# Optimization experiments

Measured on AMD Instinct MI355X. Metric: run time of the kernel, lower is better.

The kernel has to match this reference:

```python
import jax, jax.numpy as jnp
import numpy as np

EMBED_DIM = 512
SE_HIDDEN = max(1, int(EMBED_DIM * 0.25))  # 128
LN_EPS = 1e-5


def setup_inputs() -> dict:
    key = jax.random.key(0)
    ks = jax.random.split(key, 16)
    B, H, W, D = 8, 32, 32, EMBED_DIM
    s = 0.02
    return {
        "q": jax.random.normal(ks[0], (B, H, W, D), jnp.float32),
        "k": jax.random.normal(ks[1], (B, H, W, D), jnp.float32),
        "v": jax.random.normal(ks[2], (B, H, W, D), jnp.float32),
        # Linear weights stored as [in, out] (equivalent to torch W.T)
        "Wq": jax.random.normal(ks[3], (D, D), jnp.float32) * s,
        "Wk": jax.random.normal(ks[4], (D, D), jnp.float32) * s,
        "Wv": jax.random.normal(ks[5], (D, D), jnp.float32) * s,
        "Wo": jax.random.normal(ks[6], (D, D), jnp.float32) * s,
        # Conv2d kernel in HWIO layout for NHWC conv
        "conv_w": jax.random.normal(ks[7], (3, 3, D, D), jnp.float32) * s,
        "conv_b": jnp.zeros((D,), jnp.float32),
        "se_w1": jax.random.normal(ks[8], (D, SE_HIDDEN), jnp.float32) * s,
        "se_b1": jnp.zeros((SE_HIDDEN,), jnp.float32),
        "se_w2": jax.random.normal(ks[9], (SE_HIDDEN, D), jnp.float32) * s,
        "se_b2": jnp.zeros((D,), jnp.float32),
        "ln_g": jnp.ones((D,), jnp.float32),
        "ln_b": jnp.zeros((D,), jnp.float32),
    }


def _layernorm(x, g, b):
    mu = jnp.mean(x, axis=-1, keepdims=True)
    var = jnp.mean(jnp.square(x - mu), axis=-1, keepdims=True)
    return (x - mu) * jax.lax.rsqrt(var + LN_EPS) * g + b


def reference(q, k, v, Wq, Wk, Wv, Wo, conv_w, conv_b,
              se_w1, se_b1, se_w2, se_b2, ln_g, ln_b):
    B, H, W, D = q.shape
    scaler = jnp.sqrt(jnp.asarray(D, q.dtype))
    qp = q @ Wq  # [B,H,W,D]
    kp = k @ Wk
    vp = v @ Wv
    N = H * W
    qf = qp.reshape(B, N, D)
    kf = kp.reshape(B, N, D)
    vf = vp.reshape(B, N, D)
    scores = jnp.einsum('bnd,bmd->bnm', qf, kf) / scaler
    probs = jax.nn.softmax(scores, axis=-1)  # dropout p=0 -> identity
    out = jnp.einsum('bnm,bmd->bnd', probs, vf).reshape(B, H, W, D)
    out = out @ Wo
    # 3x3 same conv in NHWC
    out = jax.lax.conv_general_dilated(
        out, conv_w, window_strides=(1, 1), padding='SAME',
        dimension_numbers=('NHWC', 'HWIO', 'NHWC')) + conv_b
    # squeeze-excite: global average pool over spatial dims
    se = jnp.mean(out, axis=(1, 2))  # [B,D]
    se = jax.nn.silu(se @ se_w1 + se_b1)
    se = jax.nn.sigmoid(se @ se_w2 + se_b2)  # [B,D]
    out = out * se[:, None, None, :]
    x = qp + out  # residual uses q AFTER q_proj (q reassigned in torch code)
    return _layernorm(x, ln_g, ln_b)
```

## Files before the change

### kernel.cpp

```cpp
#include <hip/hip_runtime.h>
#include <hip/hip_bf16.h>

using bf16 = __hip_bfloat16;
typedef __attribute__((ext_vector_type(8))) short short8;
typedef __attribute__((ext_vector_type(4))) short short4v;
typedef __attribute__((ext_vector_type(4))) float f32x4;

static const size_t OFF_QP   = 0;
static const size_t OFF_KP   = (size_t)8  << 20;
static const size_t OFF_VPT  = (size_t)16 << 20;
static const size_t OFF_SC   = (size_t)24 << 20;
static const size_t OFF_WT   = (size_t)56 << 20;
static const size_t OFF_CWT  = (size_t)58 << 20;
static const size_t OFF_POOL = (size_t)63 << 20;
static const size_t OFF_SE   = ((size_t)63 << 20) + 16384;

__global__ __launch_bounds__(256) void prep_k(const float* __restrict__ Wq,
                                              const float* __restrict__ Wk,
                                              const float* __restrict__ Wv,
                                              const float* __restrict__ Wo,
                                              const float* __restrict__ convw,
                                              bf16* __restrict__ wT,
                                              bf16* __restrict__ cwT,
                                              float* __restrict__ pooled) {
    long idx = (long)blockIdx.x * 256 + threadIdx.x;
    if (idx < 4l * 262144) {
        int m = (int)(idx >> 18);
        int o = (int)(idx & 262143);
        int n = o >> 9, k = o & 511;
        const float* W = (m == 0) ? Wq : (m == 1) ? Wk : (m == 2) ? Wv : Wo;
        wT[idx] = __float2bfloat16(W[k * 512 + n]);
    } else if (idx < 4l * 262144 + 512l * 4608) {
        long o = idx - 4l * 262144;
        int co = (int)(o / 4608), t = (int)(o % 4608);
        cwT[o] = __float2bfloat16(convw[(long)t * 512 + co]);
    } else if (idx < 4l * 262144 + 512l * 4608 + 4096) {
        pooled[idx - (4l * 262144 + 512l * 4608)] = 0.f;
    }
}

template <int OP>
__global__ __launch_bounds__(256, 2) void gemm_k(
    const void* __restrict__ Ap0, const void* __restrict__ Ap1, const void* __restrict__ Ap2,
    int lda, long sA,
    const bf16* __restrict__ BT, int ldb, long sB,
    void* __restrict__ Cp, int ldc, long sC,
    int K, const float* __restrict__ bias) {
    __shared__ bf16 As[2][128 * 64];
    __shared__ bf16 Bs[2][64 * 64];
    const int tid = threadIdx.x;
    const int l = tid & 63, w = tid >> 6;
    const int wm = w >> 1, wn = w & 1;

    const int gx = gridDim.x, gy = gridDim.y;
    const int nwg = gx * gy * gridDim.z;
    const int bid = blockIdx.x + gx * (blockIdx.y + gy * blockIdx.z);
    const int swz = (bid & 7) * (nwg >> 3) + (bid >> 3);
    const int bx = swz % gx;
    const int rem = swz / gx;
    const int by = rem % gy;
    const int zb = rem / gy;

    const int m0 = by * 128, n0 = bx * 64;
    const float isc = 0.04419417382415922f;

    const bf16* Ab = nullptr;
    const float* Af = nullptr;
    if (OP == 1) {
        Af = (const float*)(zb == 0 ? Ap0 : zb == 1 ? Ap1 : Ap2);
    } else {
        Ab = (const bf16*)Ap0 + (long)zb * sA;
    }
    const bf16* Bb = BT + (OP == 1 ? (long)zb * 262144 : (long)zb * sB);

    const int fr = l & 15;
    f32x4 acc[4][2] = {};

    int pixoff[4], hh_[4], wp_[4];
    if (OP == 3) {
#pragma unroll
        for (int i = 0; i < 4; ++i) {
            int s = tid + i * 256;
            int row = s >> 3, c = s & 7;
            int p = m0 + row;
            int bb = p >> 10;
            hh_[i] = (p >> 5) & 31;
            wp_[i] = p & 31;
            pixoff[i] = ((bb * 32 + hh_[i]) * 32 + wp_[i]) * 512 + c * 8;
        }
    }

    short8 ar[4];
    float4 af0[4], af1[4];
    short8 br[2];

    auto stage_load = [&](int t) {
        int k0 = t * 64;
        int dy = 0, dx = 0, doff = 0;
        if (OP == 3) {
            int tap = k0 >> 9;
            dy = tap / 3 - 1;
            dx = tap % 3 - 1;
            doff = (dy * 32 + dx) * 512 + (k0 & 511);
        }
#pragma unroll
        for (int i = 0; i < 4; ++i) {
            int s = tid + i * 256;
            int row = s >> 3, c = s & 7;
            if (OP == 1) {
                const float* src = Af + (long)(m0 + row) * lda + k0 + c * 8;
                af0[i] = *(const float4*)src;
                af1[i] = *(const float4*)(src + 4);
            } else if (OP == 3) {
                int h2 = hh_[i] + dy, w2 = wp_[i] + dx;
                if (((unsigned)h2 < 32u) & ((unsigned)w2 < 32u)) {
                    ar[i] = *(const short8*)(Ab + pixoff[i] + doff);
                } else {
                    short8 zz = {0, 0, 0, 0, 0, 0, 0, 0};
                    ar[i] = zz;
                }
            } else {
                ar[i] = *(const short8*)(Ab + (long)(m0 + row) * lda + k0 + c * 8);
            }
        }
#pragma unroll
        for (int i = 0; i < 2; ++i) {
            int s = tid + i * 256;
            int row = s >> 3, c = s & 7;
            br[i] = *(const short8*)(Bb + (long)(n0 + row) * ldb + k0 + c * 8);
        }
    };

    auto stage_write = [&](int b) {
#pragma unroll
        for (int i = 0; i < 4; ++i) {
            int s = tid + i * 256;
            int row = s >> 3, c = s & 7;
            int cx = c ^ (row & 7);
            if (OP == 1) {
                union { short8 s8; bf16 h[8]; } u;
                u.h[0] = __float2bfloat16(af0[i].x); u.h[1] = __float2bfloat16(af0[i].y);
                u.h[2] = __float2bfloat16(af0[i].z); u.h[3] = __float2bfloat16(af0[i].w);
                u.h[4] = __float2bfloat16(af1[i].x); u.h[5] = __float2bfloat16(af1[i].y);
                u.h[6] = __float2bfloat16(af1[i].z); u.h[7] = __float2bfloat16(af1[i].w);
                *(short8*)(&As[b][row * 64 + cx * 8]) = u.s8;
            } else {
                *(short8*)(&As[b][row * 64 + cx * 8]) = ar[i];
            }
        }
#pragma unroll
        for (int i = 0; i < 2; ++i) {
            int s = tid + i * 256;
            int row = s >> 3, c = s & 7;
            int cx = c ^ (row & 7);
            *(short8*)(&Bs[b][row * 64 + cx * 8]) = br[i];
        }
    };

    auto compute = [&](int b) {
#pragma unroll
        for (int h = 0; h < 2; ++h) {
            int cx = ((l >> 4) + 4 * h) ^ (fr & 7);
            short8 afr[4], bfv[2];
#pragma unroll
            for (int m = 0; m < 4; ++m) {
                int r = wm * 64 + m * 16 + fr;
                afr[m] = *(const short8*)(&As[b][r * 64 + cx * 8]);
            }
#pragma unroll
            for (int n = 0; n < 2; ++n) {
                int r = wn * 32 + n * 16 + fr;
                bfv[n] = *(const short8*)(&Bs[b][r * 64 + cx * 8]);
            }
#pragma unroll
            for (int m = 0; m < 4; ++m)
#pragma unroll
                for (int n = 0; n < 2; ++n)
                    acc[m][n] = __builtin_amdgcn_mfma_f32_16x16x32_bf16(afr[m], bfv[n], acc[m][n], 0, 0, 0);
        }
    };

    const int nt = K >> 6;
    stage_load(0);
    stage_write(0);
    int cur = 0;
    for (int t = 0; t < nt; ++t) {
        __syncthreads();
        if (t + 1 < nt) stage_load(t + 1);
        compute(cur);
        if (t + 1 < nt) stage_write(cur ^ 1);
        cur ^= 1;
    }

    const int cr = (l >> 4) * 4, cc = l & 15;
#pragma unroll
    for (int m = 0; m < 4; ++m) {
#pragma unroll
        for (int n = 0; n < 2; ++n) {
#pragma unroll
            for (int j = 0; j < 4; ++j) {
                int r = m0 + wm * 64 + m * 16 + cr + j;
                int c = n0 + wn * 32 + n * 16 + cc;
                float vv = acc[m][n][j];
                if (OP == 3) vv += bias[c];
                if (OP == 0 || OP == 2) {
                    ((bf16*)Cp)[(long)zb * sC + (long)r * ldc + c] = __float2bfloat16(vv);
                } else if (OP == 3) {
                    ((float*)Cp)[(long)zb * sC + (long)r * ldc + c] = vv;
                } else {
                    if (zb == 2) {
                        ((bf16*)Cp)[(size_t)(OFF_VPT / 2) + ((long)(r >> 10) * 512 + c) * 1024 + (r & 1023)] =
                            __float2bfloat16(vv);
                    } else {
                        float sv = (zb == 1) ? vv * isc : vv;
                        ((bf16*)Cp)[(long)zb * 4194304 + (long)r * 512 + c] = __float2bfloat16(sv);
                    }
                }
            }
        }
    }
}

__global__ __launch_bounds__(256) void softmax_k(bf16* __restrict__ scores) {
    __shared__ float red[256];
    long row = blockIdx.x;
    bf16* base = scores + row * 1024;
    int t = threadIdx.x;
    union { short4v s4; bf16 h[4]; } u;
    u.s4 = *(const short4v*)(base + t * 4);
    float v[4];
#pragma unroll
    for (int i = 0; i < 4; ++i) v[i] = __bfloat162float(u.h[i]);
    float mx = fmaxf(fmaxf(v[0], v[1]), fmaxf(v[2], v[3]));
    red[t] = mx;
    __syncthreads();
    for (int s = 128; s > 0; s >>= 1) {
        if (t < s) red[t] = fmaxf(red[t], red[t + s]);
        __syncthreads();
    }
    mx = red[0];
    __syncthreads();
    float e[4], sum = 0.f;
#pragma unroll
    for (int i = 0; i < 4; ++i) {
        e[i] = __expf(v[i] - mx);
        sum += e[i];
    }
    red[t] = sum;
    __syncthreads();
    for (int s = 128; s > 0; s >>= 1) {
        if (t < s) red[t] += red[t + s];
        __syncthreads();
    }
    float inv = 1.0f / red[0];
#pragma unroll
    for (int i = 0; i < 4; ++i) u.h[i] = __float2bfloat16(e[i] * inv);
    *(short4v*)(base + t * 4) = u.s4;
}

__global__ __launch_bounds__(256) void pool_k(const float* __restrict__ conv_out,
                                              float* __restrict__ pooled) {
    int b = blockIdx.x, ch = blockIdx.y, ps = blockIdx.z;
    int c = ch * 256 + threadIdx.x;
    float s = 0.f;
    for (int p = ps * 128; p < ps * 128 + 128; ++p)
        s += conv_out[((long)b * 1024 + p) * 512 + c];
    atomicAdd(&pooled[b * 512 + c], s * (1.0f / 1024.0f));
}

__global__ __launch_bounds__(512) void se_mlp_k(const float* __restrict__ pooled,
                                                const float* __restrict__ w1,
                                                const float* __restrict__ b1,
                                                const float* __restrict__ w2,
                                                const float* __restrict__ b2,
                                                float* __restrict__ se) {
    __shared__ float pl[512];
    __shared__ float part[4][128];
    __shared__ float hid[128];
    const int b = blockIdx.x, t = threadIdx.x;
    pl[t] = pooled[b * 512 + t];
    __syncthreads();
    const int j = t & 127, r = t >> 7;
    float acc = 0.f;
#pragma unroll 8
    for (int s = 0; s < 128; ++s) {
        int i = r * 128 + s;
        acc += pl[i] * w1[i * 128 + j];
    }
    part[r][j] = acc;
    __syncthreads();
    if (t < 128) {
        float a = part[0][t] + part[1][t] + part[2][t] + part[3][t] + b1[t];
        hid[t] = a / (1.f + __expf(-a));
    }
    __syncthreads();
    float acc2 = b2[t];
#pragma unroll 8
    for (int jj = 0; jj < 128; ++jj)
        acc2 += hid[jj] * w2[jj * 512 + t];
    se[b * 512 + t] = 1.f / (1.f + __expf(-acc2));
}

__global__ __launch_bounds__(256) void final_k(const float* __restrict__ conv_out,
                                               const float* __restrict__ se,
                                               const bf16* __restrict__ qp,
                                               const float* __restrict__ g,
                                               const float* __restrict__ bta,
                                               float* __restrict__ out) {
    __shared__ float red[256];
    long p = blockIdx.x;
    int b = (int)(p >> 10);
    int t = threadIdx.x;
    float x[2];
#pragma unroll
    for (int i = 0; i < 2; ++i) {
        int c = t + i * 256;
        x[i] = __bfloat162float(qp[p * 512 + c]) + conv_out[p * 512 + c] * se[b * 512 + c];
    }
    red[t] = x[0] + x[1];
    __syncthreads();
    for (int s = 128; s > 0; s >>= 1) {
        if (t < s) red[t] += red[t + s];
        __syncthreads();
    }
    float mu = red[0] * (1.0f / 512.0f);
    __syncthreads();
    float d0 = x[0] - mu, d1 = x[1] - mu;
    red[t] = d0 * d0 + d1 * d1;
    __syncthreads();
    for (int s = 128; s > 0; s >>= 1) {
        if (t < s) red[t] += red[t + s];
        __syncthreads();
    }
    float inv = rsqrtf(red[0] * (1.0f / 512.0f) + 1e-5f);
#pragma unroll
    for (int i = 0; i < 2; ++i) {
        int c = t + i * 256;
        out[p * 512 + c] = (x[i] - mu) * inv * g[c] + bta[c];
    }
}

extern "C" void kernel_launch(void* const* d_in, const int* in_sizes, int n_in,
                              void* d_out, int out_size, void* d_ws, size_t ws_size,
                              hipStream_t stream) {
    const float* q      = (const float*)d_in[0];
    const float* k      = (const float*)d_in[1];
    const float* v      = (const float*)d_in[2];
    const float* Wq     = (const float*)d_in[3];
    const float* Wk     = (const float*)d_in[4];
    const float* Wv     = (const float*)d_in[5];
    const float* Wo     = (const float*)d_in[6];
    const float* convw  = (const float*)d_in[7];
    const float* convb  = (const float*)d_in[8];
    const float* se_w1  = (const float*)d_in[9];
    const float* se_b1  = (const float*)d_in[10];
    const float* se_w2  = (const float*)d_in[11];
    const float* se_b2  = (const float*)d_in[12];
    const float* ln_g   = (const float*)d_in[13];
    const float* ln_b   = (const float*)d_in[14];

    char* ws = (char*)d_ws;
    bf16*  qp     = (bf16*)(ws + OFF_QP);
    bf16*  kp     = (bf16*)(ws + OFF_KP);
    bf16*  attn   = (bf16*)(ws + OFF_KP);
    bf16*  vpT    = (bf16*)(ws + OFF_VPT);
    bf16*  out2   = (bf16*)(ws + OFF_VPT);
    bf16*  scores = (bf16*)(ws + OFF_SC);
    float* convo  = (float*)(ws + OFF_SC);
    bf16*  wT     = (bf16*)(ws + OFF_WT);
    bf16*  cwT    = (bf16*)(ws + OFF_CWT);
    float* pooled = (float*)(ws + OFF_POOL);
    float* se     = (float*)(ws + OFF_SE);

    prep_k<<<13328, 256, 0, stream>>>(Wq, Wk, Wv, Wo, convw, wT, cwT, pooled);

    gemm_k<1><<<dim3(8, 64, 3), 256, 0, stream>>>(q, k, v, 512, 0, wT, 512, 0,
                                                  ws, 512, 0, 512, nullptr);
    gemm_k<2><<<dim3(16, 8, 8), 256, 0, stream>>>(qp, nullptr, nullptr, 512, 1024l * 512,
                                                  kp, 512, 1024l * 512,
                                                  scores, 1024, 1024l * 1024, 512, nullptr);
    softmax_k<<<8192, 256, 0, stream>>>(scores);
    gemm_k<0><<<dim3(8, 8, 8), 256, 0, stream>>>(scores, nullptr, nullptr, 1024, 1024l * 1024,
                                                 vpT, 1024, 512l * 1024,
                                                 attn, 512, 1024l * 512, 1024, nullptr);
    gemm_k<0><<<dim3(8, 64, 1), 256, 0, stream>>>(attn, nullptr, nullptr, 512, 0,
                                                  wT + 3 * 262144, 512, 0,
                                                  out2, 512, 0, 512, nullptr);
    gemm_k<3><<<dim3(8, 64, 1), 256, 0, stream>>>(out2, nullptr, nullptr, 0, 0,
                                                  cwT, 4608, 0,
                                                  convo, 512, 0, 4608, convb);
    pool_k<<<dim3(8, 2, 8), 256, 0, stream>>>(convo, pooled);
    se_mlp_k<<<8, 512, 0, stream>>>(pooled, se_w1, se_b1, se_w2, se_b2, se);
    final_k<<<8192, 256, 0, stream>>>(convo, se, qp, ln_g, ln_b, (float*)d_out);
}
```

Baseline: 207.9 us.

## Load GEMM tiles directly into LDS with global_load_lds and zero-guard padding

Replaces the register-staged global-to-LDS copies for the bf16 A and B tiles with direct global_load_lds 16-byte transfers. The swizzle is now applied on the source side, and out-of-bounds conv taps read from a zeroed guard buffer. The sync moves to the end of each iteration. This aims to cut register pressure and VALU/LDS write instructions and to overlap loads with MFMA compute. The fp32 A path of the projection GEMM keeps the old register path. It relies on the per-wave LDS placement of global_load_lds matching the swizzled layout, and on the guard buffer being initialised.

```diff
diff --git a/kernel.cpp b/kernel.cpp
--- a/kernel.cpp
+++ b/kernel.cpp
@@ -6,14 +6,20 @@
 typedef __attribute__((ext_vector_type(4))) short short4v;
 typedef __attribute__((ext_vector_type(4))) float f32x4;
 
-static const size_t OFF_QP   = 0;
-static const size_t OFF_KP   = (size_t)8  << 20;
-static const size_t OFF_VPT  = (size_t)16 << 20;
-static const size_t OFF_SC   = (size_t)24 << 20;
-static const size_t OFF_WT   = (size_t)56 << 20;
-static const size_t OFF_CWT  = (size_t)58 << 20;
-static const size_t OFF_POOL = (size_t)63 << 20;
-static const size_t OFF_SE   = ((size_t)63 << 20) + 16384;
+static const size_t OFF_QP    = 0;
+static const size_t OFF_KP    = (size_t)8  << 20;
+static const size_t OFF_VPT   = (size_t)16 << 20;
+static const size_t OFF_SC    = (size_t)24 << 20;
+static const size_t OFF_WT    = (size_t)56 << 20;
+static const size_t OFF_CWT   = (size_t)58 << 20;
+static const size_t OFF_POOL  = (size_t)63 << 20;
+static const size_t OFF_SE    = ((size_t)63 << 20) + 16384;
+static const size_t OFF_GUARD = ((size_t)63 << 20) + 32768;
+
+__device__ __forceinline__ void gld16(const void* g, void* l) {
+    __builtin_amdgcn_global_load_lds((const __attribute__((address_space(1))) void*)g,
+                                     (__attribute__((address_space(3))) void*)l, 16, 0, 0);
+}
 
 __global__ __launch_bounds__(256) void prep_k(const float* __restrict__ Wq,
                                               const float* __restrict__ Wk,
@@ -22,7 +28,8 @@
                                               const float* __restrict__ convw,
                                               bf16* __restrict__ wT,
                                               bf16* __restrict__ cwT,
-                                              float* __restrict__ pooled) {
+                                              float* __restrict__ pooled,
+                                              float* __restrict__ guard) {
     long idx = (long)blockIdx.x * 256 + threadIdx.x;
     if (idx < 4l * 262144) {
         int m = (int)(idx >> 18);
@@ -34,8 +41,10 @@
         long o = idx - 4l * 262144;
         int co = (int)(o / 4608), t = (int)(o % 4608);
         cwT[o] = __float2bfloat16(convw[(long)t * 512 + co]);
-    } else if (idx < 4l * 262144 + 512l * 4608 + 4096) {
-        pooled[idx - (4l * 262144 + 512l * 4608)] = 0.f;
+    } else if (idx < 4l * 262144 + 512l * 4608 + 4096 + 256) {
+        long o = idx - (4l * 262144 + 512l * 4608);
+        if (o < 4096) pooled[o] = 0.f;
+        else guard[o - 4096] = 0.f;
     }
 }
 
@@ -49,8 +58,8 @@
     __shared__ bf16 As[2][128 * 64];
     __shared__ bf16 Bs[2][64 * 64];
     const int tid = threadIdx.x;
-    const int l = tid & 63, w = tid >> 6;
-    const int wm = w >> 1, wn = w & 1;
+    const int l = tid & 63, wv = tid >> 6;
+    const int wm = wv >> 1, wn = wv & 1;
 
     const int gx = gridDim.x, gy = gridDim.y;
     const int nwg = gx * gy * gridDim.z;
@@ -66,6 +75,7 @@
 
     const bf16* Ab = nullptr;
     const float* Af = nullptr;
+    const bf16* guard = (const bf16*)Ap1;
     if (OP == 1) {
         Af = (const float*)(zb == 0 ? Ap0 : zb == 1 ? Ap1 : Ap2);
     } else {
@@ -76,84 +86,69 @@
     const int fr = l & 15;
     f32x4 acc[4][2] = {};
 
-    int pixoff[4], hh_[4], wp_[4];
-    if (OP == 3) {
-#pragma unroll
-        for (int i = 0; i < 4; ++i) {
-            int s = tid + i * 256;
-            int row = s >> 3, c = s & 7;
-            int p = m0 + row;
-            int bb = p >> 10;
-            hh_[i] = (p >> 5) & 31;
-            wp_[i] = p & 31;
-            pixoff[i] = ((bb * 32 + hh_[i]) * 32 + wp_[i]) * 512 + c * 8;
-        }
-    }
-
-    short8 ar[4];
     float4 af0[4], af1[4];
-    short8 br[2];
-
-    auto stage_load = [&](int t) {
+
+    auto stage_issue = [&](int t, int b) {
         int k0 = t * 64;
-        int dy = 0, dx = 0, doff = 0;
-        if (OP == 3) {
-            int tap = k0 >> 9;
-            dy = tap / 3 - 1;
-            dx = tap % 3 - 1;
-            doff = (dy * 32 + dx) * 512 + (k0 & 511);
-        }
-#pragma unroll
-        for (int i = 0; i < 4; ++i) {
-            int s = tid + i * 256;
-            int row = s >> 3, c = s & 7;
-            if (OP == 1) {
+        if (OP != 1) {
+            int dy = 0, dx = 0;
+            if (OP == 3) {
+                int tap = k0 >> 9;
+                dy = tap / 3 - 1;
+                dx = tap % 3 - 1;
+            }
+#pragma unroll
+            for (int j = 0; j < 4; ++j) {
+                int s = (wv * 4 + j) * 64 + l;
+                int row = s >> 3, cx = s & 7;
+                int c = cx ^ (row & 7);
+                const bf16* src;
+                if (OP == 3) {
+                    int p = m0 + row;
+                    int bb = p >> 10, hh = (p >> 5) & 31, wp = p & 31;
+                    int h2 = hh + dy, w2 = wp + dx;
+                    int ci = (k0 & 511) + c * 8;
+                    src = (((unsigned)h2 < 32u) & ((unsigned)w2 < 32u))
+                              ? Ab + ((long)((bb * 32 + h2) * 32 + w2)) * 512 + ci
+                              : guard + (l & 63) * 8 - (l & 63) * 8;
+                    if (!(((unsigned)h2 < 32u) & ((unsigned)w2 < 32u))) src = guard;
+                } else {
+                    src = Ab + (long)(m0 + row) * lda + k0 + c * 8;
+                }
+                gld16(src, &As[b][(wv * 4 + j) * 512]);
+            }
+        } else {
+#pragma unroll
+            for (int i = 0; i < 4; ++i) {
+                int s = tid + i * 256;
+                int row = s >> 3, c = s & 7;
                 const float* src = Af + (long)(m0 + row) * lda + k0 + c * 8;
                 af0[i] = *(const float4*)src;
                 af1[i] = *(const float4*)(src + 4);
-            } else if (OP == 3) {
-                int h2 = hh_[i] + dy, w2 = wp_[i] + dx;
-                if (((unsigned)h2 < 32u) & ((unsigned)w2 < 32u)) {
-                    ar[i] = *(const short8*)(Ab + pixoff[i] + doff);
-                } else {
-                    short8 zz = {0, 0, 0, 0, 0, 0, 0, 0};
-                    ar[i] = zz;
-                }
-            } else {
-                ar[i] = *(const short8*)(Ab + (long)(m0 + row) * lda + k0 + c * 8);
-            }
-        }
-#pragma unroll
-        for (int i = 0; i < 2; ++i) {
-            int s = tid + i * 256;
-            int row = s >> 3, c = s & 7;
-            br[i] = *(const short8*)(Bb + (long)(n0 + row) * ldb + k0 + c * 8);
+            }
+        }
+#pragma unroll
+        for (int j = 0; j < 2; ++j) {
+            int s = (wv * 2 + j) * 64 + l;
+            int row = s >> 3, cx = s & 7;
+            int c = cx ^ (row & 7);
+            const bf16* src = Bb + (long)(n0 + row) * ldb + k0 + c * 8;
+            gld16(src, &Bs[b][(wv * 2 + j) * 512]);
         }
     };
 
-    auto stage_write = [&](int b) {
+    auto stage_writeA = [&](int b) {
 #pragma unroll
         for (int i = 0; i < 4; ++i) {
             int s = tid + i * 256;
             int row = s >> 3, c = s & 7;
             int cx = c ^ (row & 7);
-            if (OP == 1) {
-                union { short8 s8; bf16 h[8]; } u;
-                u.h[0] = __float2bfloat16(af0[i].x); u.h[1] = __float2bfloat16(af0[i].y);
-                u.h[2] = __float2bfloat16(af0[i].z); u.h[3] = __float2bfloat16(af0[i].w);
-                u.h[4] = __float2bfloat16(af1[i].x); u.h[5] = __float2bfloat16(af1[i].y);
-                u.h[6] = __float2bfloat16(af1[i].z); u.h[7] = __float2bfloat16(af1[i].w);
-                *(short8*)(&As[b][row * 64 + cx * 8]) = u.s8;
-            } else {
-                *(short8*)(&As[b][row * 64 + cx * 8]) = ar[i];
-            }
-        }
-#pragma unroll
-        for (int i = 0; i < 2; ++i) {
-            int s = tid + i * 256;
-            int row = s >> 3, c = s & 7;
-            int cx = c ^ (row & 7);
-            *(short8*)(&Bs[b][row * 64 + cx * 8]) = br[i];
+            union { short8 s8; bf16 h[8]; } u;
+            u.h[0] = __float2bfloat16(af0[i].x); u.h[1] = __float2bfloat16(af0[i].y);
+            u.h[2] = __float2bfloat16(af0[i].z); u.h[3] = __float2bfloat16(af0[i].w);
+            u.h[4] = __float2bfloat16(af1[i].x); u.h[5] = __float2bfloat16(af1[i].y);
+            u.h[6] = __float2bfloat16(af1[i].z); u.h[7] = __float2bfloat16(af1[i].w);
+            *(short8*)(&As[b][row * 64 + cx * 8]) = u.s8;
         }
     };
 
@@ -181,14 +176,15 @@
     };
 
     const int nt = K >> 6;
-    stage_load(0);
-    stage_write(0);
+    stage_issue(0, 0);
+    if (OP == 1) stage_writeA(0);
+    __syncthreads();
     int cur = 0;
     for (int t = 0; t < nt; ++t) {
-        __syncthreads();
-        if (t + 1 < nt) stage_load(t + 1);
+        if (t + 1 < nt) stage_issue(t + 1, cur ^ 1);
         compute(cur);
-        if (t + 1 < nt) stage_write(cur ^ 1);
+        if (OP == 1 && t + 1 < nt) stage_writeA(cur ^ 1);
+        __syncthreads();
         cur ^= 1;
     }
 
@@ -371,8 +367,9 @@
     bf16*  cwT    = (bf16*)(ws + OFF_CWT);
     float* pooled = (float*)(ws + OFF_POOL);
     float* se     = (float*)(ws + OFF_SE);
-
-    prep_k<<<13328, 256, 0, stream>>>(Wq, Wk, Wv, Wo, convw, wT, cwT, pooled);
+    float* guard  = (float*)(ws + OFF_GUARD);
+
+    prep_k<<<13329, 256, 0, stream>>>(Wq, Wk, Wv, Wo, convw, wT, cwT, pooled, guard);
 
     gemm_k<1><<<dim3(8, 64, 3), 256, 0, stream>>>(q, k, v, 512, 0, wT, 512, 0,
                                                   ws, 512, 0, 512, nullptr);
@@ -386,7 +383,7 @@
     gemm_k<0><<<dim3(8, 64, 1), 256, 0, stream>>>(attn, nullptr, nullptr, 512, 0,
                                                   wT + 3 * 262144, 512, 0,
                                                   out2, 512, 0, 512, nullptr);
-    gemm_k<3><<<dim3(8, 64, 1), 256, 0, stream>>>(out2, nullptr, nullptr, 0, 0,
+    gemm_k<3><<<dim3(8, 64, 1), 256, 0, stream>>>(out2, guard, nullptr, 0, 0,
                                                   cwT, 4608, 0,
                                                   convo, 512, 0, 4608, convb);
     pool_k<<<dim3(8, 2, 8), 256, 0, stream>>>(convo, pooled);
```

Measured after the change: 220.7 us. 1.06x slower.

## Deepen GEMM global-load prefetch to four register stages ahead

Applied to the files above, without the earlier changes.

The GEMM main loop now keeps four sets of staging registers and issues global loads three to four K-tiles ahead of the tile being computed, instead of one tile ahead. Shared memory stays double-buffered. The intent is to hide more global-memory latency behind the MFMA work. The cost is many more live registers per thread (the fp32 path in particular), which can lower occupancy or cause spills. The loop also assumes the tile count is a multiple of four and that at least four tiles exist.

```diff
diff --git a/kernel.cpp b/kernel.cpp
--- a/kernel.cpp
+++ b/kernel.cpp
@@ -90,11 +90,14 @@
         }
     }
 
-    short8 ar[4];
-    float4 af0[4], af1[4];
-    short8 br[2];
-
-    auto stage_load = [&](int t) {
+    struct SR {
+        short8 ar[4];
+        float4 af0[4], af1[4];
+        short8 br[2];
+    };
+    SR S0, S1, S2, S3;
+
+    auto stage_load = [&](int t, SR& S) {
         int k0 = t * 64;
         int dy = 0, dx = 0, doff = 0;
         if (OP == 3) {
@@ -109,29 +112,29 @@
             int row = s >> 3, c = s & 7;
             if (OP == 1) {
                 const float* src = Af + (long)(m0 + row) * lda + k0 + c * 8;
-                af0[i] = *(const float4*)src;
-                af1[i] = *(const float4*)(src + 4);
+                S.af0[i] = *(const float4*)src;
+                S.af1[i] = *(const float4*)(src + 4);
             } else if (OP == 3) {
                 int h2 = hh_[i] + dy, w2 = wp_[i] + dx;
                 if (((unsigned)h2 < 32u) & ((unsigned)w2 < 32u)) {
-                    ar[i] = *(const short8*)(Ab + pixoff[i] + doff);
+                    S.ar[i] = *(const short8*)(Ab + pixoff[i] + doff);
                 } else {
                     short8 zz = {0, 0, 0, 0, 0, 0, 0, 0};
-                    ar[i] = zz;
+                    S.ar[i] = zz;
                 }
             } else {
-                ar[i] = *(const short8*)(Ab + (long)(m0 + row) * lda + k0 + c * 8);
+                S.ar[i] = *(const short8*)(Ab + (long)(m0 + row) * lda + k0 + c * 8);
             }
         }
 #pragma unroll
         for (int i = 0; i < 2; ++i) {
             int s = tid + i * 256;
             int row = s >> 3, c = s & 7;
-            br[i] = *(const short8*)(Bb + (long)(n0 + row) * ldb + k0 + c * 8);
+            S.br[i] = *(const short8*)(Bb + (long)(n0 + row) * ldb + k0 + c * 8);
         }
     };
 
-    auto stage_write = [&](int b) {
+    auto stage_write = [&](int b, SR& S) {
 #pragma unroll
         for (int i = 0; i < 4; ++i) {
             int s = tid + i * 256;
@@ -139,13 +142,13 @@
             int cx = c ^ (row & 7);
             if (OP == 1) {
                 union { short8 s8; bf16 h[8]; } u;
-                u.h[0] = __float2bfloat16(af0[i].x); u.h[1] = __float2bfloat16(af0[i].y);
-                u.h[2] = __float2bfloat16(af0[i].z); u.h[3] = __float2bfloat16(af0[i].w);
-                u.h[4] = __float2bfloat16(af1[i].x); u.h[5] = __float2bfloat16(af1[i].y);
-                u.h[6] = __float2bfloat16(af1[i].z); u.h[7] = __float2bfloat16(af1[i].w);
+                u.h[0] = __float2bfloat16(S.af0[i].x); u.h[1] = __float2bfloat16(S.af0[i].y);
+                u.h[2] = __float2bfloat16(S.af0[i].z); u.h[3] = __float2bfloat16(S.af0[i].w);
+                u.h[4] = __float2bfloat16(S.af1[i].x); u.h[5] = __float2bfloat16(S.af1[i].y);
+                u.h[6] = __float2bfloat16(S.af1[i].z); u.h[7] = __float2bfloat16(S.af1[i].w);
                 *(short8*)(&As[b][row * 64 + cx * 8]) = u.s8;
             } else {
-                *(short8*)(&As[b][row * 64 + cx * 8]) = ar[i];
+                *(short8*)(&As[b][row * 64 + cx * 8]) = S.ar[i];
             }
         }
 #pragma unroll
@@ -153,7 +156,7 @@
             int s = tid + i * 256;
             int row = s >> 3, c = s & 7;
             int cx = c ^ (row & 7);
-            *(short8*)(&Bs[b][row * 64 + cx * 8]) = br[i];
+            *(short8*)(&Bs[b][row * 64 + cx * 8]) = S.br[i];
         }
     };
 
@@ -181,15 +184,28 @@
     };
 
     const int nt = K >> 6;
-    stage_load(0);
-    stage_write(0);
-    int cur = 0;
-    for (int t = 0; t < nt; ++t) {
-        __syncthreads();
-        if (t + 1 < nt) stage_load(t + 1);
-        compute(cur);
-        if (t + 1 < nt) stage_write(cur ^ 1);
-        cur ^= 1;
+    stage_load(0, S0);
+    stage_load(1, S1);
+    stage_load(2, S2);
+    stage_load(3, S3);
+    stage_write(0, S0);
+    for (int t = 0; t < nt; t += 4) {
+        __syncthreads();
+        if (t + 4 < nt) stage_load(t + 4, S0);
+        compute(0);
+        stage_write(1, S1);
+        __syncthreads();
+        if (t + 5 < nt) stage_load(t + 5, S1);
+        compute(1);
+        stage_write(0, S2);
+        __syncthreads();
+        if (t + 6 < nt) stage_load(t + 6, S2);
+        compute(0);
+        stage_write(1, S3);
+        __syncthreads();
+        if (t + 7 < nt) stage_load(t + 7, S3);
+        compute(1);
+        if (t + 4 < nt) stage_write(0, S0);
     }
 
     const int cr = (l >> 4) * 4, cc = l & 15;
```

Measured after the change: 207.5 us. About the same (-0.2%).

## Widen GEMM tiles to 128x128, fuse SE pooling into conv epilogue, store conv in bf16

Applied to the files above, without the earlier changes.

Enlarges the GEMM block tile from 128x64 to 128x128, so each wave computes a 64x64 sub-tile with 16 MFMA accumulators, which improves operand reuse out of LDS and halves the grid sizes. The conv GEMM epilogue now accumulates per-column sums and atomically adds them into the pooled buffer, which removes the separate pool kernel. It also writes the conv output in bf16 rather than fp32, which halves the traffic for the final layernorm pass. In exchange there is higher register and LDS pressure that may lower occupancy at launch_bounds(256,2), fewer blocks to fill the GPU, and a small precision loss on the conv output.

```diff
diff --git a/kernel.cpp b/kernel.cpp
--- a/kernel.cpp
+++ b/kernel.cpp
@@ -45,9 +45,9 @@
     int lda, long sA,
     const bf16* __restrict__ BT, int ldb, long sB,
     void* __restrict__ Cp, int ldc, long sC,
-    int K, const float* __restrict__ bias) {
+    int K, const float* __restrict__ bias, float* __restrict__ pooled) {
     __shared__ bf16 As[2][128 * 64];
-    __shared__ bf16 Bs[2][64 * 64];
+    __shared__ bf16 Bs[2][128 * 64];
     const int tid = threadIdx.x;
     const int l = tid & 63, w = tid >> 6;
     const int wm = w >> 1, wn = w & 1;
@@ -61,7 +61,7 @@
     const int by = rem % gy;
     const int zb = rem / gy;
 
-    const int m0 = by * 128, n0 = bx * 64;
+    const int m0 = by * 128, n0 = bx * 128;
     const float isc = 0.04419417382415922f;
 
     const bf16* Ab = nullptr;
@@ -74,7 +74,7 @@
     const bf16* Bb = BT + (OP == 1 ? (long)zb * 262144 : (long)zb * sB);
 
     const int fr = l & 15;
-    f32x4 acc[4][2] = {};
+    f32x4 acc[4][4] = {};
 
     int pixoff[4], hh_[4], wp_[4];
     if (OP == 3) {
@@ -92,7 +92,7 @@
 
     short8 ar[4];
     float4 af0[4], af1[4];
-    short8 br[2];
+    short8 br[4];
 
     auto stage_load = [&](int t) {
         int k0 = t * 64;
@@ -124,7 +124,7 @@
             }
         }
 #pragma unroll
-        for (int i = 0; i < 2; ++i) {
+        for (int i = 0; i < 4; ++i) {
             int s = tid + i * 256;
             int row = s >> 3, c = s & 7;
             br[i] = *(const short8*)(Bb + (long)(n0 + row) * ldb + k0 + c * 8);
@@ -149,7 +149,7 @@
             }
         }
 #pragma unroll
-        for (int i = 0; i < 2; ++i) {
+        for (int i = 0; i < 4; ++i) {
             int s = tid + i * 256;
             int row = s >> 3, c = s & 7;
             int cx = c ^ (row & 7);
@@ -161,21 +161,21 @@
 #pragma unroll
         for (int h = 0; h < 2; ++h) {
             int cx = ((l >> 4) + 4 * h) ^ (fr & 7);
-            short8 afr[4], bfv[2];
+            short8 afr[4], bfv[4];
 #pragma unroll
             for (int m = 0; m < 4; ++m) {
                 int r = wm * 64 + m * 16 + fr;
                 afr[m] = *(const short8*)(&As[b][r * 64 + cx * 8]);
             }
 #pragma unroll
-            for (int n = 0; n < 2; ++n) {
-                int r = wn * 32 + n * 16 + fr;
+            for (int n = 0; n < 4; ++n) {
+                int r = wn * 64 + n * 16 + fr;
                 bfv[n] = *(const short8*)(&Bs[b][r * 64 + cx * 8]);
             }
 #pragma unroll
             for (int m = 0; m < 4; ++m)
 #pragma unroll
-                for (int n = 0; n < 2; ++n)
+                for (int n = 0; n < 4; ++n)
                     acc[m][n] = __builtin_amdgcn_mfma_f32_16x16x32_bf16(afr[m], bfv[n], acc[m][n], 0, 0, 0);
         }
     };
@@ -193,20 +193,22 @@
     }
 
     const int cr = (l >> 4) * 4, cc = l & 15;
+    float csum[4] = {0.f, 0.f, 0.f, 0.f};
 #pragma unroll
     for (int m = 0; m < 4; ++m) {
 #pragma unroll
-        for (int n = 0; n < 2; ++n) {
+        for (int n = 0; n < 4; ++n) {
 #pragma unroll
             for (int j = 0; j < 4; ++j) {
                 int r = m0 + wm * 64 + m * 16 + cr + j;
-                int c = n0 + wn * 32 + n * 16 + cc;
+                int c = n0 + wn * 64 + n * 16 + cc;
                 float vv = acc[m][n][j];
-                if (OP == 3) vv += bias[c];
-                if (OP == 0 || OP == 2) {
+                if (OP == 3) {
+                    vv += bias[c];
+                    csum[n] += vv;
+                    ((bf16*)Cp)[(long)r * ldc + c] = __float2bfloat16(vv);
+                } else if (OP == 0 || OP == 2) {
                     ((bf16*)Cp)[(long)zb * sC + (long)r * ldc + c] = __float2bfloat16(vv);
-                } else if (OP == 3) {
-                    ((float*)Cp)[(long)zb * sC + (long)r * ldc + c] = vv;
                 } else {
                     if (zb == 2) {
                         ((bf16*)Cp)[(size_t)(OFF_VPT / 2) + ((long)(r >> 10) * 512 + c) * 1024 + (r & 1023)] =
@@ -219,6 +221,14 @@
             }
         }
     }
+    if (OP == 3) {
+        int bb = m0 >> 10;
+#pragma unroll
+        for (int n = 0; n < 4; ++n) {
+            int c = n0 + wn * 64 + n * 16 + cc;
+            atomicAdd(&pooled[bb * 512 + c], csum[n] * (1.0f / 1024.0f));
+        }
+    }
 }
 
 __global__ __launch_bounds__(256) void softmax_k(bf16* __restrict__ scores) {
@@ -256,16 +266,6 @@
 #pragma unroll
     for (int i = 0; i < 4; ++i) u.h[i] = __float2bfloat16(e[i] * inv);
     *(short4v*)(base + t * 4) = u.s4;
-}
-
-__global__ __launch_bounds__(256) void pool_k(const float* __restrict__ conv_out,
-                                              float* __restrict__ pooled) {
-    int b = blockIdx.x, ch = blockIdx.y, ps = blockIdx.z;
-    int c = ch * 256 + threadIdx.x;
-    float s = 0.f;
-    for (int p = ps * 128; p < ps * 128 + 128; ++p)
-        s += conv_out[((long)b * 1024 + p) * 512 + c];
-    atomicAdd(&pooled[b * 512 + c], s * (1.0f / 1024.0f));
 }
 
 __global__ __launch_bounds__(512) void se_mlp_k(const float* __restrict__ pooled,
@@ -301,7 +301,7 @@
     se[b * 512 + t] = 1.f / (1.f + __expf(-acc2));
 }
 
-__global__ __launch_bounds__(256) void final_k(const float* __restrict__ conv_out,
+__global__ __launch_bounds__(256) void final_k(const bf16* __restrict__ conv_out,
                                                const float* __restrict__ se,
                                                const bf16* __restrict__ qp,
                                                const float* __restrict__ g,
@@ -315,7 +315,8 @@
 #pragma unroll
     for (int i = 0; i < 2; ++i) {
         int c = t + i * 256;
-        x[i] = __bfloat162float(qp[p * 512 + c]) + conv_out[p * 512 + c] * se[b * 512 + c];
+        x[i] = __bfloat162float(qp[p * 512 + c]) +
+               __bfloat162float(conv_out[p * 512 + c]) * se[b * 512 + c];
     }
     red[t] = x[0] + x[1];
     __syncthreads();
@@ -366,7 +367,7 @@
     bf16*  vpT    = (bf16*)(ws + OFF_VPT);
     bf16*  out2   = (bf16*)(ws + OFF_VPT);
     bf16*  scores = (bf16*)(ws + OFF_SC);
-    float* convo  = (float*)(ws + OFF_SC);
+    bf16*  convo  = (bf16*)(ws + OFF_SC);
     bf16*  wT     = (bf16*)(ws + OFF_WT);
     bf16*  cwT    = (bf16*)(ws + OFF_CWT);
     float* pooled = (float*)(ws + OFF_POOL);
@@ -374,22 +375,21 @@
 
     prep_k<<<13328, 256, 0, stream>>>(Wq, Wk, Wv, Wo, convw, wT, cwT, pooled);
 
-    gemm_k<1><<<dim3(8, 64, 3), 256, 0, stream>>>(q, k, v, 512, 0, wT, 512, 0,
-                                                  ws, 512, 0, 512, nullptr);
-    gemm_k<2><<<dim3(16, 8, 8), 256, 0, stream>>>(qp, nullptr, nullptr, 512, 1024l * 512,
-                                                  kp, 512, 1024l * 512,
-                                                  scores, 1024, 1024l * 1024, 512, nullptr);
+    gemm_k<1><<<dim3(4, 64, 3), 256, 0, stream>>>(q, k, v, 512, 0, wT, 512, 0,
+                                                  ws, 512, 0, 512, nullptr, nullptr);
+    gemm_k<2><<<dim3(8, 8, 8), 256, 0, stream>>>(qp, nullptr, nullptr, 512, 1024l * 512,
+                                                 kp, 512, 1024l * 512,
+                                                 scores, 1024, 1024l * 1024, 512, nullptr, nullptr);
     softmax_k<<<8192, 256, 0, stream>>>(scores);
-    gemm_k<0><<<dim3(8, 8, 8), 256, 0, stream>>>(scores, nullptr, nullptr, 1024, 1024l * 1024,
+    gemm_k<0><<<dim3(4, 8, 8), 256, 0, stream>>>(scores, nullptr, nullptr, 1024, 1024l * 1024,
                                                  vpT, 1024, 512l * 1024,
-                                                 attn, 512, 1024l * 512, 1024, nullptr);
-    gemm_k<0><<<dim3(8, 64, 1), 256, 0, stream>>>(attn, nullptr, nullptr, 512, 0,
+                                                 attn, 512, 1024l * 512, 1024, nullptr, nullptr);
+    gemm_k<0><<<dim3(4, 64, 1), 256, 0, stream>>>(attn, nullptr, nullptr, 512, 0,
                                                   wT + 3 * 262144, 512, 0,
-                                                  out2, 512, 0, 512, nullptr);
-    gemm_k<3><<<dim3(8, 64, 1), 256, 0, stream>>>(out2, nullptr, nullptr, 0, 0,
+                                                  out2, 512, 0, 512, nullptr, nullptr);
+    gemm_k<3><<<dim3(4, 64, 1), 256, 0, stream>>>(out2, nullptr, nullptr, 0, 0,
                                                   cwT, 4608, 0,
-                                                  convo, 512, 0, 4608, convb);
-    pool_k<<<dim3(8, 2, 8), 256, 0, stream>>>(convo, pooled);
+                                                  convo, 512, 0, 4608, convb, pooled);
     se_mlp_k<<<8, 512, 0, stream>>>(pooled, se_w1, se_b1, se_w2, se_b2, se);
     final_k<<<8192, 256, 0, stream>>>(convo, se, qp, ln_g, ln_b, (float*)d_out);
 }
```

Result: slower. 213.1 us (+2.5%).
